# Kernel tuning notes

Hardware: AMD Instinct MI355X
Metric: run time of the kernel (lower is better)

The kernel has to match this reference:

```python
import jax, jax.numpy as jnp
import numpy as np
import math

D_MODEL = 2048
N_HEADS = 16
HEAD_DIM = D_MODEL // N_HEADS


def setup_inputs() -> dict:
    key = jax.random.key(0)
    k1, k2, k3, k4 = jax.random.split(key, 4)
    bs, seq = 2, 2048
    x = jax.random.normal(k1, (bs, seq, D_MODEL), dtype=jnp.float32)
    # torch nn.Linear weights are [out, in]; y = x @ W.T
    scale_q = 1.0 / math.sqrt(D_MODEL)
    Wq = jax.random.uniform(k2, (D_MODEL, D_MODEL), jnp.float32, -scale_q, scale_q)
    Wkv = jax.random.uniform(k3, (2 * HEAD_DIM, D_MODEL), jnp.float32, -scale_q, scale_q)
    Wo = jax.random.uniform(k4, (D_MODEL, D_MODEL), jnp.float32, -scale_q, scale_q)
    return {"x": x, "Wq": Wq, "Wkv": Wkv, "Wo": Wo}


def reference(x, Wq, Wkv, Wo):
    bs, seq, _ = x.shape
    q = x @ Wq.T                      # [b, s, d_model]
    kv = x @ Wkv.T                    # [b, s, 2*head_dim]
    k, v = jnp.split(kv, 2, axis=-1)  # each [b, s, head_dim] (single shared KV head)
    q = q.reshape(bs, seq, N_HEADS, HEAD_DIM).transpose(0, 2, 1, 3)  # [b, h, s, d]
    # MQA: broadcast shared K/V across heads via einsum (no explicit expand)
    attn = jnp.einsum("bhqd,bkd->bhqk", q, k) / math.sqrt(HEAD_DIM)  # [b, h, s, s]
    causal = jnp.tril(jnp.ones((seq, seq), dtype=bool))
    attn = jnp.where(causal[None, None], attn, jnp.float32(-1e9))
    attn = jax.nn.softmax(attn, axis=-1)
    out = jnp.einsum("bhqk,bkd->bhqd", attn, v)                      # [b, h, s, d]
    out = out.transpose(0, 2, 1, 3).reshape(bs, seq, D_MODEL)
    return out @ Wo.T
```

## Files before the change

kernel.cpp:

```cpp
#include <hip/hip_runtime.h>
#include <hip/hip_bf16.h>

typedef __attribute__((ext_vector_type(8))) short bf16x8;
typedef __attribute__((ext_vector_type(4))) float f32x4;
typedef __attribute__((ext_vector_type(16))) float f32x16;
typedef __attribute__((ext_vector_type(4))) ushort u16x4;

#define AS1 __attribute__((address_space(1)))
#define AS3 __attribute__((address_space(3)))

static __device__ __forceinline__ ushort f2b(float f) {
    union { float f; unsigned u; } v;
    v.f = f;
    unsigned r = v.u + 0x7FFF + ((v.u >> 16) & 1);
    return (ushort)(r >> 16);
}

__global__ __launch_bounds__(256) void cvt_all(const float* __restrict__ x,
                                               const float* __restrict__ Wq,
                                               const float* __restrict__ Wkv,
                                               const float* __restrict__ Wo,
                                               ushort* __restrict__ xb,
                                               ushort* __restrict__ wqkvb,
                                               ushort* __restrict__ wob)
{
    int i = blockIdx.x * blockDim.x + threadIdx.x;
    const int stride = gridDim.x * blockDim.x;
    for (; i < 4325376; i += stride) {
        const float4* src; ushort4* dst; int j;
        if (i < 2097152)      { src = (const float4*)x;   dst = (ushort4*)xb;              j = i; }
        else if (i < 3145728) { src = (const float4*)Wq;  dst = (ushort4*)wqkvb;           j = i - 2097152; }
        else if (i < 3276800) { src = (const float4*)Wkv; dst = (ushort4*)wqkvb + 1048576; j = i - 3145728; }
        else                  { src = (const float4*)Wo;  dst = (ushort4*)wob;             j = i - 3276800; }
        float4 v = src[j];
        ushort4 o; o.x = f2b(v.x); o.y = f2b(v.y); o.z = f2b(v.z); o.w = f2b(v.w);
        dst[j] = o;
    }
}

template<bool F32OUT>
__global__ __launch_bounds__(256) void gemm_bt(const ushort* __restrict__ A,
                                               const ushort* __restrict__ B,
                                               void* __restrict__ Cv,
                                               int M, int N, int K)
{
    __shared__ ushort As[2][128 * 32];
    __shared__ ushort Bs[2][128 * 32];
    const int tid  = threadIdx.x;
    const int lane = tid & 63;
    const int wid  = tid >> 6;
    const int l15  = lane & 15;
    const int lg   = lane >> 4;
    const int nwg8 = gridDim.x >> 3;
    const int kblk = blockIdx.x;
    const int swz  = (kblk & 7) * nwg8 + (kblk >> 3);
    const int nx   = N >> 7;
    const int brow = (swz / nx) * 128;
    const int bcol = (swz % nx) * 128;
    const int wr = wid >> 1, wc = wid & 1;

    f32x4 acc[4][4] = {};

    auto stage = [&](int bi, int k0) {
        const ushort* Ap = A + (size_t)brow * K + k0;
        const ushort* Bp = B + (size_t)bcol * K + k0;
#pragma unroll
        for (int j = 0; j < 2; ++j) {
            const int ci = wid * 2 + j;
            const int G  = ci * 64 + lane;
            const int r  = G >> 2, gc = G & 3;
            const int sgc = gc ^ ((r >> 1) & 3);
            __builtin_amdgcn_global_load_lds(
                (const AS1 void*)(Ap + (size_t)r * K + sgc * 8),
                (AS3 void*)(&As[bi][ci * 512]), 16, 0, 0);
            __builtin_amdgcn_global_load_lds(
                (const AS1 void*)(Bp + (size_t)r * K + sgc * 8),
                (AS3 void*)(&Bs[bi][ci * 512]), 16, 0, 0);
        }
    };

    stage(0, 0);
    __syncthreads();
    int cur = 0;

    for (int k0 = 0; k0 < K; k0 += 32) {
        if (k0 + 32 < K) stage(cur ^ 1, k0 + 32);

        bf16x8 af[4], bfr[4];
#pragma unroll
        for (int m = 0; m < 4; ++m) {
            int row = wr * 64 + m * 16 + l15;
            int slot = lg ^ ((row >> 1) & 3);
            af[m] = *(const bf16x8*)(&As[cur][row * 32 + slot * 8]);
        }
#pragma unroll
        for (int n = 0; n < 4; ++n) {
            int row = wc * 64 + n * 16 + l15;
            int slot = lg ^ ((row >> 1) & 3);
            bfr[n] = *(const bf16x8*)(&Bs[cur][row * 32 + slot * 8]);
        }
#pragma unroll
        for (int m = 0; m < 4; ++m)
#pragma unroll
            for (int n = 0; n < 4; ++n)
                acc[m][n] = __builtin_amdgcn_mfma_f32_16x16x32_bf16(af[m], bfr[n], acc[m][n], 0, 0, 0);

        __syncthreads();
        cur ^= 1;
    }

#pragma unroll
    for (int m = 0; m < 4; ++m)
#pragma unroll
        for (int n = 0; n < 4; ++n) {
            int row0 = brow + wr * 64 + m * 16 + lg * 4;
            int col  = bcol + wc * 64 + n * 16 + l15;
#pragma unroll
            for (int j = 0; j < 4; ++j) {
                float v = acc[m][n][j];
                if (F32OUT)
                    ((float*)Cv)[(size_t)(row0 + j) * N + col] = v;
                else
                    ((ushort*)Cv)[(size_t)(row0 + j) * N + col] = f2b(v);
            }
        }
}

#define VMW4 asm volatile("s_waitcnt vmcnt(4)" ::: "memory")
#define VMW0 asm volatile("s_waitcnt vmcnt(0)" ::: "memory")
#define QKV_PHASE(BUF, MH, NH, STG, DRN) do {                                            \
    if (NH == 0) {                                                                       \
        _Pragma("unroll")                                                                \
        for (int m = 0; m < 4; ++m) {                                                    \
            _Pragma("unroll")                                                            \
            for (int kh = 0; kh < 2; ++kh) {                                             \
                int r  = MH * 128 + wr * 64 + m * 16 + l15;                              \
                int sl = (kh * 4 + lg) ^ (r & 7);                                        \
                af[m][kh] = *(const bf16x8*)(&Asm[BUF][r * 64 + sl * 8]);                \
            }                                                                            \
        }                                                                                \
    }                                                                                    \
    _Pragma("unroll")                                                                    \
    for (int n = 0; n < 2; ++n) {                                                        \
        _Pragma("unroll")                                                                \
        for (int kh = 0; kh < 2; ++kh) {                                                 \
            int r  = NH * 128 + wc * 32 + n * 16 + l15;                                  \
            int sl = (kh * 4 + lg) ^ (r & 7);                                            \
            bf[n][kh] = *(const bf16x8*)(&Bsm[BUF][r * 64 + sl * 8]);                    \
        }                                                                                \
    }                                                                                    \
    STG;                                                                                 \
    __builtin_amdgcn_s_barrier();                                                        \
    asm volatile("s_waitcnt lgkmcnt(0)" ::: "memory");                                   \
    __builtin_amdgcn_s_setprio(1);                                                       \
    _Pragma("unroll")                                                                    \
    for (int m = 0; m < 4; ++m) {                                                        \
        _Pragma("unroll")                                                                \
        for (int n = 0; n < 2; ++n) {                                                    \
            acc[MH * 4 + m][NH * 2 + n] = __builtin_amdgcn_mfma_f32_16x16x32_bf16(       \
                af[m][0], bf[n][0], acc[MH * 4 + m][NH * 2 + n], 0, 0, 0);               \
            acc[MH * 4 + m][NH * 2 + n] = __builtin_amdgcn_mfma_f32_16x16x32_bf16(       \
                af[m][1], bf[n][1], acc[MH * 4 + m][NH * 2 + n], 0, 0, 0);               \
        }                                                                                \
    }                                                                                    \
    __builtin_amdgcn_s_setprio(0);                                                       \
    DRN;                                                                                 \
    __builtin_amdgcn_s_barrier();                                                        \
} while (0)

__global__ __launch_bounds__(512, 2) void gemm_qkv8(const ushort* __restrict__ A,
                                                    const ushort* __restrict__ B,
                                                    ushort* __restrict__ Cq,
                                                    ushort* __restrict__ Ckv,
                                                    ushort* __restrict__ Vt)
{
    constexpr int K = 2048;
    __shared__ ushort Asm[2][16384];
    __shared__ ushort Bsm[2][16384];

    const int tid  = threadIdx.x;
    const int lane = tid & 63;
    const int wid  = tid >> 6;
    const int l15  = lane & 15;
    const int lg   = lane >> 4;
    const int wr   = wid >> 2;
    const int wc   = wid & 3;
    const int bid  = blockIdx.x;
    const int swz  = (bid & 7) * 18 + (bid >> 3);
    const int brow = (swz / 9) * 256;
    const int bcol = (swz % 9) * 256;

    f32x4  acc[8][4] = {};
    bf16x8 af[4][2], bf[2][2];

    auto stageH = [&](int bi, int which, int t) {
        const int k0 = t << 6;
        const ushort* src;
        ushort* dst;
        if (which == 0)      { src = A + (size_t)brow * K + k0;         dst = &Asm[bi][0];    }
        else if (which == 1) { src = A + (size_t)(brow + 128) * K + k0; dst = &Asm[bi][8192]; }
        else if (which == 2) { src = B + (size_t)bcol * K + k0;         dst = &Bsm[bi][0];    }
        else                 { src = B + (size_t)(bcol + 128) * K + k0; dst = &Bsm[bi][8192]; }
#pragma unroll
        for (int j = 0; j < 2; ++j) {
            const int t8 = j * 512 + tid;
            const int r  = t8 >> 3;
            const int s  = (t8 & 7) ^ (r & 7);
            __builtin_amdgcn_global_load_lds(
                (const AS1 void*)(src + (size_t)r * K + s * 8),
                (AS3 void*)(dst + (j * 512 + (wid << 6)) * 8), 16, 0, 0);
        }
    };

    stageH(0, 0, 0); stageH(0, 2, 0); stageH(0, 1, 0); stageH(0, 3, 0);
    stageH(1, 0, 1); stageH(1, 2, 1);
    VMW4;
    __builtin_amdgcn_s_barrier();

#pragma unroll 1
    for (int i = 0; i < 15; ++i) {
        const int t1 = 2 * i + 1;
        QKV_PHASE(0, 0, 0, { stageH(1, 1, t1); stageH(1, 3, t1); }, ((void)0));
        QKV_PHASE(0, 0, 1, { stageH(0, 0, t1 + 1); },               ((void)0));
        QKV_PHASE(0, 1, 0, { ((void)0); },                          ((void)0));
        QKV_PHASE(0, 1, 1, { stageH(0, 2, t1 + 1); },               VMW4);
        QKV_PHASE(1, 0, 0, { stageH(0, 1, t1 + 1); stageH(0, 3, t1 + 1); }, ((void)0));
        QKV_PHASE(1, 0, 1, { stageH(1, 0, t1 + 2); },               ((void)0));
        QKV_PHASE(1, 1, 0, { ((void)0); },                          ((void)0));
        QKV_PHASE(1, 1, 1, { stageH(1, 2, t1 + 2); },               VMW4);
    }
    QKV_PHASE(0, 0, 0, { stageH(1, 1, 31); stageH(1, 3, 31); }, ((void)0));
    QKV_PHASE(0, 0, 1, { ((void)0); }, ((void)0));
    QKV_PHASE(0, 1, 0, { ((void)0); }, ((void)0));
    QKV_PHASE(0, 1, 1, { ((void)0); }, VMW0);
    QKV_PHASE(1, 0, 0, { ((void)0); }, ((void)0));
    QKV_PHASE(1, 0, 1, { ((void)0); }, ((void)0));
    QKV_PHASE(1, 1, 0, { ((void)0); }, ((void)0));
    QKV_PHASE(1, 1, 1, { ((void)0); }, ((void)0));

#pragma unroll
    for (int MH = 0; MH < 2; ++MH)
#pragma unroll
    for (int m = 0; m < 4; ++m)
#pragma unroll
    for (int NH = 0; NH < 2; ++NH)
#pragma unroll
    for (int n = 0; n < 2; ++n) {
        const int row0 = brow + MH * 128 + wr * 64 + m * 16 + lg * 4;
        const int col  = bcol + NH * 128 + wc * 32 + n * 16 + l15;
        const f32x4 v4 = acc[MH * 4 + m][NH * 2 + n];
#pragma unroll
        for (int j = 0; j < 4; ++j) {
            const float v = v4[j];
            const int row = row0 + j;
            if (col < 2048) {
                Cq[(size_t)row * 2048 + col] = f2b(v);
            } else if (col < 2176) {
                Ckv[(size_t)row * 256 + (col - 2048)] = f2b(v);
            } else {
                Vt[((size_t)((row >> 11) * 128 + (col - 2176))) * 2048 + (row & 2047)] = f2b(v);
            }
        }
    }
}

__global__ __launch_bounds__(256, 2) void mqa_attn12(const ushort* __restrict__ Q,
                                                     const ushort* __restrict__ KV,
                                                     const ushort* __restrict__ Vt,
                                                     ushort* __restrict__ O)
{
    const int tid = threadIdx.x, lane = tid & 63, wid = tid >> 6;
    const int c31 = lane & 31, H = lane >> 5;
    const int bid = blockIdx.x;
    const int a  = bid & 31;
    const int hp = (bid >> 5) & 7;
    const int b  = bid >> 8;
    const int h  = hp * 2 + (wid >> 1);
    const int p  = wid & 1;

    __shared__ __align__(16) ushort SMEM[32768];

    const ushort* KVb = KV + (size_t)b * 2048 * 256;
    const ushort* Vtb = Vt + (size_t)b * 128 * 2048;
    const float C2 = 0.12751763f;
    const float mC = 32.0f * C2;

    auto stageK = [&](int buf, int par, int t) {
        ushort* dst = SMEM + (buf * 2 + par) * 4096;
        const int kvb = t * 32;
#pragma unroll
        for (int i = 0; i < 8; ++i) {
            int G = i * 64 + lane;
            int r = G >> 4, gc = G & 15;
            int sgc = gc ^ (r & 15);
            __builtin_amdgcn_global_load_lds(
                (const AS1 void*)(KVb + (size_t)(kvb + r) * 256 + sgc * 8),
                (AS3 void*)(dst + i * 512), 16, 0, 0);
        }
    };
    auto stageV = [&](int buf, int par, int t) {
        ushort* dst = SMEM + 16384 + (buf * 2 + par) * 4096;
        const int kvb = t * 32;
#pragma unroll
        for (int i = 0; i < 8; ++i) {
            int G = i * 64 + lane;
            int g = G >> 3, s = G & 7;
            int u = s ^ (g & 7);
            int r = 2 * g + (u & 1);
            int cc = u >> 1;
            __builtin_amdgcn_global_load_lds(
                (const AS1 void*)(Vtb + (size_t)r * 2048 + kvb + cc * 8),
                (AS3 void*)(dst + G * 8), 16, 0, 0);
        }
    };

#pragma unroll 1
    for (int phase = 0; phase < 2; ++phase) {
        const int tile  = phase ? (63 - a) : a;
        const int qtile = tile * 32;
        const int U = tile + 1;
        const int S = (U + 1) >> 1;
        const size_t qrow = (size_t)(b * 2048 + qtile + c31);

        bf16x8 qf[8];
#pragma unroll
        for (int dk = 0; dk < 8; ++dk)
            qf[dk] = *(const bf16x8*)(Q + qrow * 2048 + h * 128 + dk * 16 + H * 8);

        float l_run = 0.f;
        f32x16 of[4];
#pragma unroll
        for (int dt = 0; dt < 4; ++dt)
#pragma unroll
            for (int r = 0; r < 16; ++r) of[dt][r] = 0.f;

        {
            int t = p;
            if (t < U) { if (wid < 2) stageK(0, p, t); else stageV(0, p, t); }
        }
        __syncthreads();

#pragma unroll 1
        for (int s = 0; s < S; ++s) {
            if (s + 1 < S) {
                int tn = 2 * (s + 1) + p;
                if (tn < U) { if (wid < 2) stageK((s + 1) & 1, p, tn); else stageV((s + 1) & 1, p, tn); }
            }
            const int t = 2 * s + p;
            if (t < U) {
                const ushort* Kb = SMEM + ((s & 1) * 2 + p) * 4096;
                const ushort* Vb = SMEM + 16384 + ((s & 1) * 2 + p) * 4096;
                const bool maskt = (t == tile);

                f32x16 sg = {0,0,0,0,0,0,0,0,0,0,0,0,0,0,0,0};
                __builtin_amdgcn_s_setprio(1);
#pragma unroll
                for (int dk = 0; dk < 8; ++dk) {
                    bf16x8 kf = *(const bf16x8*)(Kb + c31 * 128 + ((dk * 16 + H * 8) ^ ((c31 & 15) << 3)));
                    sg = __builtin_amdgcn_mfma_f32_32x32x16_bf16(kf, qf[dk], sg, 0, 0, 0);
                }
                __builtin_amdgcn_s_setprio(0);

                float e[16];
#pragma unroll
                for (int r = 0; r < 16; ++r) {
                    float v = sg[r];
                    if (maskt) {
                        int crow = (r & 3) + 8 * (r >> 2) + 4 * H;
                        if (crow > c31) v = -1e30f;
                    }
                    e[r] = __builtin_amdgcn_exp2f(__builtin_fmaf(v, C2, -mC));
                }
                float rsum = 0.f;
#pragma unroll
                for (int r = 0; r < 16; ++r) rsum += e[r];
                rsum += __shfl_xor(rsum, 32);
                l_run += rsum;

                unsigned pk[8];
#pragma unroll
                for (int i = 0; i < 8; ++i)
                    asm("v_cvt_pk_bf16_f32 %0, %1, %2" : "=v"(pk[i]) : "v"(e[2 * i]), "v"(e[2 * i + 1]));
                asm("v_permlane32_swap_b32 %0, %1" : "+v"(pk[0]), "+v"(pk[2]));
                asm("v_permlane32_swap_b32 %0, %1" : "+v"(pk[1]), "+v"(pk[3]));
                asm("v_permlane32_swap_b32 %0, %1" : "+v"(pk[4]), "+v"(pk[6]));
                asm("v_permlane32_swap_b32 %0, %1" : "+v"(pk[5]), "+v"(pk[7]));
                union { unsigned u[4]; bf16x8 v; } P0, P1;
                P0.u[0] = pk[0]; P0.u[1] = pk[1]; P0.u[2] = pk[2]; P0.u[3] = pk[3];
                P1.u[0] = pk[4]; P1.u[1] = pk[5]; P1.u[2] = pk[6]; P1.u[3] = pk[7];

                __builtin_amdgcn_s_setprio(1);
#pragma unroll
                for (int dt = 0; dt < 4; ++dt) {
                    int g  = dt * 16 + (c31 >> 1);
                    int sw = g & 7;
                    int b0 = c31 & 1;
                    int s0 = (2 * H + b0) ^ sw;
                    int s1 = (4 + 2 * H + b0) ^ sw;
                    bf16x8 v0 = *(const bf16x8*)(Vb + (g * 8 + s0) * 8);
                    bf16x8 v1 = *(const bf16x8*)(Vb + (g * 8 + s1) * 8);
                    of[dt] = __builtin_amdgcn_mfma_f32_32x32x16_bf16(v0, P0.v, of[dt], 0, 0, 0);
                    of[dt] = __builtin_amdgcn_mfma_f32_32x32x16_bf16(v1, P1.v, of[dt], 0, 0, 0);
                }
                __builtin_amdgcn_s_setprio(0);
            }
            __syncthreads();
        }

        float* mlb = (float*)SMEM;
        if (H == 0) mlb[wid * 32 + c31] = l_run;
        __syncthreads();
        {
            float lo = mlb[(wid ^ 1) * 32 + c31];
            float inv = 1.0f / (l_run + lo);
            float* ob = (float*)(SMEM + 512) + (wid >> 1) * 4096;
            if (p == 1) {
#pragma unroll
                for (int dt = 0; dt < 4; ++dt)
#pragma unroll
                    for (int rq = 0; rq < 4; ++rq) {
                        f32x4 w;
#pragma unroll
                        for (int j = 0; j < 4; ++j) w[j] = of[dt][rq * 4 + j];
                        *(f32x4*)(ob + ((dt * 4 + rq) * 64 + lane) * 4) = w;
                    }
            }
            __syncthreads();
            if (p == 0) {
                ushort* Orow = O + qrow * 2048 + h * 128;
#pragma unroll
                for (int dt = 0; dt < 4; ++dt)
#pragma unroll
                    for (int rq = 0; rq < 4; ++rq) {
                        f32x4 r4 = *(const f32x4*)(ob + ((dt * 4 + rq) * 64 + lane) * 4);
                        u16x4 o4;
#pragma unroll
                        for (int j = 0; j < 4; ++j)
                            o4[j] = f2b((of[dt][rq * 4 + j] + r4[j]) * inv);
                        int d0 = dt * 32 + rq * 8 + 4 * H;
                        *(u16x4*)(Orow + d0) = o4;
                    }
            }
        }
        __syncthreads();
    }
}

extern "C" void kernel_launch(void* const* d_in, const int* in_sizes, int n_in,
                              void* d_out, int out_size, void* d_ws, size_t ws_size,
                              hipStream_t stream) {
    const float* x   = (const float*)d_in[0];
    const float* Wq  = (const float*)d_in[1];
    const float* Wkv = (const float*)d_in[2];
    const float* Wo  = (const float*)d_in[3];

    char* ws = (char*)d_ws;
    ushort* xb    = (ushort*)(ws);
    ushort* wqkvb = (ushort*)(ws + 16777216);
    ushort* wob   = (ushort*)(ws + 35651584);
    ushort* qb    = (ushort*)(ws + 44040192);
    ushort* kvb   = (ushort*)(ws + 60817408);
    ushort* vtb   = (ushort*)(ws + 62914560);
    ushort* aob   = xb;

    cvt_all<<<2048, 256, 0, stream>>>(x, Wq, Wkv, Wo, xb, wqkvb, wob);

    gemm_qkv8<<<144, 512, 0, stream>>>(xb, wqkvb, qb, kvb, vtb);
    mqa_attn12<<<512, 256, 0, stream>>>(qb, kvb, vtb, aob);
    gemm_bt<true><<<512, 256, 0, stream>>>(aob, wob, d_out, 4096, 2048, 2048);
}
```

Before: 189.9 us.

## Widen gemm_bt K-tile to 64 and reschedule QKV GEMM prefetch stages

The generic bt GEMM (likely the output projection) now stages 64-wide K slices with an 8-slot XOR swizzle, doing two MFMAs per barrier and halving the number of K iterations and syncs. The QKV GEMM pipeline issues one A-half stage earlier, redistributes prefetches across phases, and waits with vmcnt(3) instead of vmcnt(4). Scheduling barriers are added so the compiler cannot move the LDS reads and MFMAs across the staging code. This doubles shared memory in gemm_bt, which may reduce occupancy.

```diff
diff --git a/kernel.cpp b/kernel.cpp
--- a/kernel.cpp
+++ b/kernel.cpp
@@ -44,8 +44,8 @@
                                                void* __restrict__ Cv,
                                                int M, int N, int K)
 {
-    __shared__ ushort As[2][128 * 32];
-    __shared__ ushort Bs[2][128 * 32];
+    __shared__ ushort As[2][128 * 64];
+    __shared__ ushort Bs[2][128 * 64];
     const int tid  = threadIdx.x;
     const int lane = tid & 63;
     const int wid  = tid >> 6;
@@ -65,17 +65,17 @@
         const ushort* Ap = A + (size_t)brow * K + k0;
         const ushort* Bp = B + (size_t)bcol * K + k0;
 #pragma unroll
-        for (int j = 0; j < 2; ++j) {
-            const int ci = wid * 2 + j;
-            const int G  = ci * 64 + lane;
-            const int r  = G >> 2, gc = G & 3;
-            const int sgc = gc ^ ((r >> 1) & 3);
+        for (int j = 0; j < 4; ++j) {
+            const int G = j * 256 + tid;
+            const int r = G >> 3;
+            const int s = (G & 7) ^ (r & 7);
+            const int dc = (j * 256 + (wid << 6)) * 8;
             __builtin_amdgcn_global_load_lds(
-                (const AS1 void*)(Ap + (size_t)r * K + sgc * 8),
-                (AS3 void*)(&As[bi][ci * 512]), 16, 0, 0);
+                (const AS1 void*)(Ap + (size_t)r * K + s * 8),
+                (AS3 void*)(&As[bi][dc]), 16, 0, 0);
             __builtin_amdgcn_global_load_lds(
-                (const AS1 void*)(Bp + (size_t)r * K + sgc * 8),
-                (AS3 void*)(&Bs[bi][ci * 512]), 16, 0, 0);
+                (const AS1 void*)(Bp + (size_t)r * K + s * 8),
+                (AS3 void*)(&Bs[bi][dc]), 16, 0, 0);
         }
     };
 
@@ -83,27 +83,35 @@
     __syncthreads();
     int cur = 0;
 
-    for (int k0 = 0; k0 < K; k0 += 32) {
-        if (k0 + 32 < K) stage(cur ^ 1, k0 + 32);
-
-        bf16x8 af[4], bfr[4];
+    for (int k0 = 0; k0 < K; k0 += 64) {
+        if (k0 + 64 < K) stage(cur ^ 1, k0 + 64);
+
+        bf16x8 af[4][2], bfr[4][2];
 #pragma unroll
         for (int m = 0; m < 4; ++m) {
             int row = wr * 64 + m * 16 + l15;
-            int slot = lg ^ ((row >> 1) & 3);
-            af[m] = *(const bf16x8*)(&As[cur][row * 32 + slot * 8]);
+#pragma unroll
+            for (int kh = 0; kh < 2; ++kh) {
+                int sl = (kh * 4 + lg) ^ (row & 7);
+                af[m][kh] = *(const bf16x8*)(&As[cur][row * 64 + sl * 8]);
+            }
         }
 #pragma unroll
         for (int n = 0; n < 4; ++n) {
             int row = wc * 64 + n * 16 + l15;
-            int slot = lg ^ ((row >> 1) & 3);
-            bfr[n] = *(const bf16x8*)(&Bs[cur][row * 32 + slot * 8]);
+#pragma unroll
+            for (int kh = 0; kh < 2; ++kh) {
+                int sl = (kh * 4 + lg) ^ (row & 7);
+                bfr[n][kh] = *(const bf16x8*)(&Bs[cur][row * 64 + sl * 8]);
+            }
         }
 #pragma unroll
         for (int m = 0; m < 4; ++m)
 #pragma unroll
-            for (int n = 0; n < 4; ++n)
-                acc[m][n] = __builtin_amdgcn_mfma_f32_16x16x32_bf16(af[m], bfr[n], acc[m][n], 0, 0, 0);
+            for (int n = 0; n < 4; ++n) {
+                acc[m][n] = __builtin_amdgcn_mfma_f32_16x16x32_bf16(af[m][0], bfr[n][0], acc[m][n], 0, 0, 0);
+                acc[m][n] = __builtin_amdgcn_mfma_f32_16x16x32_bf16(af[m][1], bfr[n][1], acc[m][n], 0, 0, 0);
+            }
 
         __syncthreads();
         cur ^= 1;
@@ -126,7 +134,7 @@
         }
 }
 
-#define VMW4 asm volatile("s_waitcnt vmcnt(4)" ::: "memory")
+#define VMW3 asm volatile("s_waitcnt vmcnt(3)" ::: "memory")
 #define VMW0 asm volatile("s_waitcnt vmcnt(0)" ::: "memory")
 #define QKV_PHASE(BUF, MH, NH, STG, DRN) do {                                            \
     if (NH == 0) {                                                                       \
@@ -149,9 +157,11 @@
             bf[n][kh] = *(const bf16x8*)(&Bsm[BUF][r * 64 + sl * 8]);                    \
         }                                                                                \
     }                                                                                    \
+    __builtin_amdgcn_sched_barrier(0);              \
     STG;                                                                                 \
     __builtin_amdgcn_s_barrier();                                                        \
     asm volatile("s_waitcnt lgkmcnt(0)" ::: "memory");                                   \
+    __builtin_amdgcn_sched_barrier(0);          \
     __builtin_amdgcn_s_setprio(1);                                                       \
     _Pragma("unroll")                                                                    \
     for (int m = 0; m < 4; ++m) {                                                        \
@@ -213,23 +223,23 @@
     };
 
     stageH(0, 0, 0); stageH(0, 2, 0); stageH(0, 1, 0); stageH(0, 3, 0);
-    stageH(1, 0, 1); stageH(1, 2, 1);
-    VMW4;
+    stageH(1, 0, 1); stageH(1, 2, 1); stageH(1, 1, 1);
+    VMW3;
     __builtin_amdgcn_s_barrier();
 
 #pragma unroll 1
     for (int i = 0; i < 15; ++i) {
         const int t1 = 2 * i + 1;
-        QKV_PHASE(0, 0, 0, { stageH(1, 1, t1); stageH(1, 3, t1); }, ((void)0));
-        QKV_PHASE(0, 0, 1, { stageH(0, 0, t1 + 1); },               ((void)0));
-        QKV_PHASE(0, 1, 0, { ((void)0); },                          ((void)0));
-        QKV_PHASE(0, 1, 1, { stageH(0, 2, t1 + 1); },               VMW4);
-        QKV_PHASE(1, 0, 0, { stageH(0, 1, t1 + 1); stageH(0, 3, t1 + 1); }, ((void)0));
-        QKV_PHASE(1, 0, 1, { stageH(1, 0, t1 + 2); },               ((void)0));
-        QKV_PHASE(1, 1, 0, { ((void)0); },                          ((void)0));
-        QKV_PHASE(1, 1, 1, { stageH(1, 2, t1 + 2); },               VMW4);
+        QKV_PHASE(0, 0, 0, { stageH(1, 3, t1); },                    ((void)0));
+        QKV_PHASE(0, 0, 1, { stageH(0, 0, t1 + 1); },                ((void)0));
+        QKV_PHASE(0, 1, 0, { ((void)0); },                           ((void)0));
+        QKV_PHASE(0, 1, 1, { stageH(0, 2, t1 + 1); stageH(0, 1, t1 + 1); }, VMW3);
+        QKV_PHASE(1, 0, 0, { stageH(0, 3, t1 + 1); },                ((void)0));
+        QKV_PHASE(1, 0, 1, { stageH(1, 0, t1 + 2); },                ((void)0));
+        QKV_PHASE(1, 1, 0, { ((void)0); },                           ((void)0));
+        QKV_PHASE(1, 1, 1, { stageH(1, 2, t1 + 2); stageH(1, 1, t1 + 2); }, VMW3);
     }
-    QKV_PHASE(0, 0, 0, { stageH(1, 1, 31); stageH(1, 3, 31); }, ((void)0));
+    QKV_PHASE(0, 0, 0, { stageH(1, 3, 31); }, ((void)0));
     QKV_PHASE(0, 0, 1, { ((void)0); }, ((void)0));
     QKV_PHASE(0, 1, 0, { ((void)0); }, ((void)0));
     QKV_PHASE(0, 1, 1, { ((void)0); }, VMW0);
```

Result: faster. 180.1 us (-5.2%).
